# Performance work log

Measured on AMD Instinct MI355X. Metric: run time of the kernel, lower is better.

Reference implementation:

```python
import jax, jax.numpy as jnp
import numpy as np

EMB = 2048; H = 32; G = 8; D = 64; GS = H // G; EPS = 1e-6

def _rmsnorm(x, scale):
    x32 = x.astype(jnp.float32)
    var = jnp.mean(x32 * x32, axis=-1, keepdims=True)
    return (x32 * jax.lax.rsqrt(var + EPS) * scale).astype(x.dtype)

def _rope(x, cos, sin):
    # x: [B, h, S, D]; cos/sin: [S, D]
    d = x.shape[-1]
    x1, x2 = x[..., : d // 2], x[..., d // 2 :]
    rot = jnp.concatenate([-x2, x1], axis=-1)
    return (x * cos[None, None] + rot * sin[None, None]).astype(x.dtype)

def setup_inputs() -> dict:
    key = jax.random.key(0)
    ks = jax.random.split(key, 6)
    B, S = 2, 2048
    x = jax.random.normal(ks[0], (B, S, EMB), jnp.float32)
    # causal mask: True = blocked (masked_fill semantics)
    mask = jnp.triu(jnp.ones((S, S), dtype=bool), k=1)
    # standard RoPE tables, half-dim rotation, shape [S, D]
    inv_freq = 1.0 / (10000.0 ** (jnp.arange(0, D, 2, dtype=jnp.float32) / D))
    ang = jnp.arange(S, dtype=jnp.float32)[:, None] * inv_freq[None, :]  # [S, D/2]
    cos = jnp.concatenate([jnp.cos(ang), jnp.cos(ang)], axis=-1)
    sin = jnp.concatenate([jnp.sin(ang), jnp.sin(ang)], axis=-1)
    Wq = jax.random.normal(ks[1], (EMB, H * D), jnp.float32) * 0.02
    Wk = jax.random.normal(ks[2], (EMB, G * D), jnp.float32) * 0.02
    Wv = jax.random.normal(ks[3], (EMB, G * D), jnp.float32) * 0.02
    Wo = jax.random.normal(ks[4], (H * D, EMB), jnp.float32) * 0.02
    q_scale = jnp.ones((D,), jnp.float32)
    k_scale = jnp.ones((D,), jnp.float32)
    return {"x": x, "mask": mask, "cos": cos, "sin": sin, "Wq": Wq, "Wk": Wk,
            "Wv": Wv, "Wo": Wo, "q_scale": q_scale, "k_scale": k_scale}

def reference(x, mask, cos, sin, Wq, Wk, Wv, Wo, q_scale, k_scale):
    B, S, _ = x.shape
    q = (x @ Wq).reshape(B, S, H, D).transpose(0, 2, 1, 3)  # [B,H,S,D]
    k = (x @ Wk).reshape(B, S, G, D).transpose(0, 2, 1, 3)  # [B,G,S,D]
    v = (x @ Wv).reshape(B, S, G, D).transpose(0, 2, 1, 3)
    q = _rmsnorm(q, q_scale)
    k = _rmsnorm(k, k_scale)
    q = _rope(q, cos, sin)
    k = _rope(k, cos, sin)
    # GQA expansion (repeat_interleave over head dim)
    k = jnp.repeat(k, GS, axis=1)
    v = jnp.repeat(v, GS, axis=1)
    scale = 1.0 / np.float32(np.sqrt(D))
    s = jnp.einsum('bhqd,bhkd->bhqk', q.astype(jnp.float32), k.astype(jnp.float32)) * scale
    # flash path is causal regardless of `mask` arg; mask here equals causal
    s = jnp.where(mask[None, None], -jnp.inf, s)
    w = jax.nn.softmax(s, axis=-1)
    ctx = jnp.einsum('bhqk,bhkd->bhqd', w, v.astype(jnp.float32))
    ctx = ctx.transpose(0, 2, 1, 3).reshape(B, S, H * D)
    return ctx @ Wo
```

## Files before the change

### kernel.cpp

```cpp
#include <hip/hip_runtime.h>
#include <hip/hip_bf16.h>
#include <cstdint>
#include <cstddef>

#define EMB   2048
#define NH_   32
#define NG_   8
#define DH_   64
#define SEQ_  2048
#define BB_   2
#define MTOT  4096
#define LDQKV 3072
#define SM_C  0.18033688f

typedef __attribute__((ext_vector_type(8))) short s16x8;
typedef __attribute__((ext_vector_type(8))) unsigned short u16x8;
typedef __attribute__((ext_vector_type(4))) float f32x4;
typedef __attribute__((ext_vector_type(16))) float f32x16;
typedef __attribute__((ext_vector_type(4))) unsigned int u32x4;
typedef __attribute__((ext_vector_type(2))) unsigned int u32x2;
typedef __attribute__((ext_vector_type(2))) int i32x2;

__device__ __forceinline__ float bf2f(unsigned short u) {
  unsigned int x = (unsigned int)u << 16; return __uint_as_float(x);
}
__device__ __forceinline__ unsigned short f2bf(float f) {
  unsigned int x = __float_as_uint(f);
  x = x + 0x7FFFu + ((x >> 16) & 1u);
  return (unsigned short)(x >> 16);
}
__device__ __forceinline__ float ninf() { return __int_as_float(0xff800000); }
__device__ __forceinline__ unsigned int pack_bf2(float a, float b) {
  unsigned int r;
  asm("v_cvt_pk_bf16_f32 %0, %1, %2" : "=v"(r) : "v"(a), "v"(b));
  return r;
}
__device__ __forceinline__ void plswap(unsigned int& a, unsigned int& b) {
  i32x2 r = __builtin_amdgcn_permlane32_swap((int)a, (int)b, false, false);
  a = (unsigned int)r[0]; b = (unsigned int)r[1];
}
__device__ __forceinline__ void plswapf(float& a, float& b) {
  unsigned int ua = __float_as_uint(a), ub = __float_as_uint(b);
  plswap(ua, ub);
  a = __uint_as_float(ua); b = __uint_as_float(ub);
}

__device__ __forceinline__ void glds16(const void* g, void* l) {
  __builtin_amdgcn_global_load_lds((const __attribute__((address_space(1))) void*)g,
                                   (__attribute__((address_space(3))) void*)l, 16, 0, 0);
}

__device__ __forceinline__ void hw_sincos(float ang, float& c, float& s) {
  float rev = ang * 0.15915494309f;
  rev = rev - floorf(rev);
  asm("v_cos_f32 %0, %1" : "=v"(c) : "v"(rev));
  asm("v_sin_f32 %0, %1" : "=v"(s) : "v"(rev));
}

__global__ __launch_bounds__(256)
void prep(const float* __restrict__ x, const float* __restrict__ Wq,
          const float* __restrict__ Wk, const float* __restrict__ Wv,
          const float* __restrict__ Wo, unsigned short* __restrict__ xb,
          unsigned short* __restrict__ Wt, unsigned short* __restrict__ Wot) {
  __shared__ float tile[64][65];
  const int tid = threadIdx.x;
  const int bid = blockIdx.x;
  if (bid < 4096) {
    size_t i = (size_t)bid * 256 + tid;
    float4 a = *(const float4*)(x + i * 8);
    float4 c = *(const float4*)(x + i * 8 + 4);
    u16x8 o;
    o[0] = f2bf(a.x); o[1] = f2bf(a.y); o[2] = f2bf(a.z); o[3] = f2bf(a.w);
    o[4] = f2bf(c.x); o[5] = f2bf(c.y); o[6] = f2bf(c.z); o[7] = f2bf(c.w);
    *(u16x8*)(xb + i * 8) = o;
    return;
  }
  const float* in; unsigned short* out; int N; int local;
  if (bid < 5120)      { in = Wq; out = Wt;                       N = 2048; local = bid - 4096; }
  else if (bid < 5376) { in = Wk; out = Wt + (size_t)2048 * 2048; N = 512;  local = bid - 5120; }
  else if (bid < 5632) { in = Wv; out = Wt + (size_t)2560 * 2048; N = 512;  local = bid - 5376; }
  else                 { in = Wo; out = Wot;                      N = 2048; local = bid - 5632; }
  const int ntile = N >> 6;
  const int n0 = (local % ntile) * 64, k0 = (local / ntile) * 64;
  #pragma unroll
  for (int jj = 0; jj < 4; ++jj) {
    int r = (tid >> 4) + jj * 16;
    int c = (tid & 15) * 4;
    float4 v = *(const float4*)(in + (size_t)(k0 + r) * N + n0 + c);
    tile[r][c] = v.x; tile[r][c + 1] = v.y; tile[r][c + 2] = v.z; tile[r][c + 3] = v.w;
  }
  __syncthreads();
  #pragma unroll
  for (int rep = 0; rep < 2; ++rep) {
    int u = rep * 256 + tid;
    int nl = u >> 3, ch = u & 7;
    u16x8 o;
    #pragma unroll
    for (int e = 0; e < 8; ++e) o[e] = f2bf(tile[ch * 8 + e][nl]);
    *(u16x8*)(out + (size_t)(n0 + nl) * 2048 + k0 + ch * 8) = o;
  }
}

template<int BN, int F32OUT>
__global__ __launch_bounds__(512, 1)
void gemm256(const unsigned short* __restrict__ A, const unsigned short* __restrict__ Bt,
             void* __restrict__ C, int ldc) {
  constexpr int BUF = 16384 + BN * 64;
  constexpr int WN = BN / 64;
  constexpr int RW = 256 / (8 / WN);
  __shared__ __align__(16) char L[4][BUF];
  const int tid = threadIdx.x;
  const int wid = tid >> 6, lane = tid & 63;
  const int wm = wid / WN, wn = wid % WN;
  const int grp = lane >> 4, l15 = lane & 15;
  const int bm = blockIdx.y * 256, bn = blockIdx.x * BN;
  const int nt = 64;

  const int srow = tid >> 2;
  const int sc = (tid & 3) ^ ((srow >> 1) & 3);
  const int grp2 = grp ^ ((l15 >> 1) & 3);

  auto stage_ht = [&](int t, int h) {
    const unsigned short* src = (h < 2)
      ? A  + (size_t)(bm + h * 128 + srow) * 2048 + t * 32 + sc * 8
      : Bt + (size_t)(bn + (h - 2) * 128 + srow) * 2048 + t * 32 + sc * 8;
    glds16(src, &L[t & 3][h * 8192 + wid * 1024]);
  };

  constexpr int NST = 2 + BN / 128;
  f32x4 acc[RW / 16][4] = {};

  #pragma unroll
  for (int h = 0; h < NST; ++h) stage_ht(0, h);
  #pragma unroll
  for (int h = 0; h < NST; ++h) stage_ht(1, h);
  if constexpr (BN == 256) asm volatile("s_waitcnt vmcnt(4)" ::: "memory");
  else                     asm volatile("s_waitcnt vmcnt(3)" ::: "memory");
  __builtin_amdgcn_sched_barrier(0);
  __builtin_amdgcn_s_barrier();
  __builtin_amdgcn_sched_barrier(0);

  for (int t = 0; t < nt; ++t) {
    const char* Ab = &L[t & 3][0]     + (size_t)(wm * RW + l15) * 64 + grp2 * 16;
    const char* Bb = &L[t & 3][16384] + (size_t)(wn * 64 + l15) * 64 + grp2 * 16;
    const bool pre = (t + 2 < nt);
    if (pre) { stage_ht(t + 2, 0); stage_ht(t + 2, 1); }
    s16x8 bf[4], af[4];
    #pragma unroll
    for (int j = 0; j < 4; ++j) bf[j] = *(const s16x8*)(Bb + j * 1024);
    #pragma unroll
    for (int i = 0; i < 4; ++i) af[i] = *(const s16x8*)(Ab + i * 1024);
    __builtin_amdgcn_s_setprio(1);
    #pragma unroll
    for (int i = 0; i < 4; ++i)
      #pragma unroll
      for (int j = 0; j < 4; ++j)
        acc[i][j] = __builtin_amdgcn_mfma_f32_16x16x32_bf16(af[i], bf[j], acc[i][j], 0, 0, 0);
    __builtin_amdgcn_s_setprio(0);
    if constexpr (BN == 256) {
      if (pre) { stage_ht(t + 2, 2); stage_ht(t + 2, 3); }
      #pragma unroll
      for (int i = 0; i < 4; ++i) af[i] = *(const s16x8*)(Ab + (4 + i) * 1024);
      __builtin_amdgcn_s_setprio(1);
      #pragma unroll
      for (int i = 0; i < 4; ++i)
        #pragma unroll
        for (int j = 0; j < 4; ++j)
          acc[4 + i][j] = __builtin_amdgcn_mfma_f32_16x16x32_bf16(af[i], bf[j], acc[4 + i][j], 0, 0, 0);
      __builtin_amdgcn_s_setprio(0);
    } else {
      if (pre) stage_ht(t + 2, 2);
    }
    if (t + 1 < nt) {
      if (pre) {
        if constexpr (BN == 256) asm volatile("s_waitcnt vmcnt(4)" ::: "memory");
        else                     asm volatile("s_waitcnt vmcnt(3)" ::: "memory");
      } else {
        asm volatile("s_waitcnt vmcnt(0)" ::: "memory");
      }
      __builtin_amdgcn_sched_barrier(0);
      __builtin_amdgcn_s_barrier();
      __builtin_amdgcn_sched_barrier(0);
    }
  }

  #pragma unroll
  for (int i = 0; i < RW / 16; ++i)
    #pragma unroll
    for (int j = 0; j < 4; ++j)
      #pragma unroll
      for (int r = 0; r < 4; ++r) {
        int row = bm + wm * RW + i * 16 + grp * 4 + r;
        int col = bn + wn * 64 + j * 16 + l15;
        float v = acc[i][j][r];
        if (F32OUT) ((float*)C)[(size_t)row * ldc + col] = v;
        else        ((unsigned short*)C)[(size_t)row * ldc + col] = f2bf(v);
      }
}

__global__ __launch_bounds__(256)
void kvtile_rms(const unsigned short* __restrict__ qkv, const float* __restrict__ ksc,
                const float* __restrict__ cs, const float* __restrict__ sn,
                unsigned short* __restrict__ Kt, unsigned short* __restrict__ Vt) {
  __shared__ unsigned short Kl[32][72];
  __shared__ unsigned short Vl[32][72];
  const int tid = threadIdx.x;
  const int kt = blockIdx.x;
  const int bg = blockIdx.y;
  const int b = bg >> 3, g = bg & 7;
  {
    const int row = tid >> 3, ch = tid & 7;
    const int spos = kt * 32 + row;
    u16x8 kv = *(const u16x8*)(qkv + (size_t)(b * SEQ_ + spos) * LDQKV + 2048 + g * 64 + ch * 8);
    float v[8]; float sq = 0.f;
    #pragma unroll
    for (int e = 0; e < 8; ++e) { v[e] = bf2f(kv[e]); sq += v[e] * v[e]; }
    sq += __shfl_xor(sq, 1); sq += __shfl_xor(sq, 2); sq += __shfl_xor(sq, 4);
    const float rn = rsqrtf(sq * (1.f / 64.f) + 1e-6f);
    float xn[8];
    #pragma unroll
    for (int e = 0; e < 8; ++e) xn[e] = v[e] * rn * ksc[ch * 8 + e];
    float pn[8];
    #pragma unroll
    for (int e = 0; e < 8; ++e) pn[e] = __shfl_xor(xn[e], 4);
    const bool lo = (ch < 4);
    #pragma unroll
    for (int e = 0; e < 8; ++e) {
      int d = ch * 8 + e;
      float c = cs[spos * 64 + d], si = sn[spos * 64 + d];
      float o = lo ? (xn[e] * c - pn[e] * si) : fmaf(xn[e], c, pn[e] * si);
      Kl[row][d] = f2bf(o);
    }
    u16x8 vv = *(const u16x8*)(qkv + (size_t)(b * SEQ_ + spos) * LDQKV + 2560 + g * 64 + ch * 8);
    #pragma unroll
    for (int e = 0; e < 8; ++e) Vl[row][ch * 8 + e] = vv[e];
  }
  __syncthreads();
  {
    int c = tid >> 5, row = tid & 31;
    u16x8 o;
    #pragma unroll
    for (int e = 0; e < 8; ++e) o[e] = Kl[row][c * 8 + e];
    *(u16x8*)(Kt + (((size_t)(bg * 64 + kt)) << 11) + (c * 32 + row) * 8) = o;
  }
  {
    int c = tid >> 6, d = tid & 63;
    u16x8 o;
    #pragma unroll
    for (int e = 0; e < 8; ++e) o[e] = Vl[c * 8 + e][d];
    *(u16x8*)(Vt + (((size_t)(bg * 64 + kt)) << 11) + (c * 64 + d) * 8) = o;
  }
}

__global__ __launch_bounds__(256)
void attn_mfma14(const unsigned short* __restrict__ qkv, const float* __restrict__ qsc,
                 const unsigned short* __restrict__ Ktg, const unsigned short* __restrict__ Vtg,
                 unsigned short* __restrict__ ctx) {
  __shared__ __align__(16) unsigned short LR[16 * 1024];
  const int tid = threadIdx.x;
  const int w = tid >> 6, lane = tid & 63;
  const int l31 = lane & 31, half = lane >> 5;
  const int bid = blockIdx.x;
  const int x8 = bid & 7, r = bid >> 3;
  const int bg = x8 + 8 * (r & 1);
  const int rr = r >> 1;
  const int slot = rr >> 4, gi = rr & 15;
  const int qt = (slot == 0) ? (63 - gi) : (slot == 1) ? gi
               : (slot == 2) ? (47 - gi) : (16 + gi);
  const int b = bg >> 3, g = bg & 7, h = g * 4 + w;
  const int qbase = qt * 32;
  const int nkt = qt + 1;

  s16x8 qf[4];
  {
    const int spos = qbase + l31;
    float qv[4][8]; float sq = 0.f;
    #pragma unroll
    for (int s2 = 0; s2 < 4; ++s2) {
      u16x8 raw = *(const u16x8*)(qkv + (size_t)(b * SEQ_ + spos) * LDQKV + h * 64 + half * 8 + s2 * 16);
      #pragma unroll
      for (int e = 0; e < 8; ++e) { qv[s2][e] = bf2f(raw[e]); sq += qv[s2][e] * qv[s2][e]; }
    }
    sq += __shfl_xor(sq, 32);
    const float rn = rsqrtf(sq * (1.f / 64.f) + 1e-6f);
    float xn[4][8];
    #pragma unroll
    for (int s2 = 0; s2 < 4; ++s2)
      #pragma unroll
      for (int e = 0; e < 8; ++e) xn[s2][e] = qv[s2][e] * rn * qsc[s2 * 16 + half * 8 + e];
    const float fs = (float)spos;
    float qo[4][8];
    #pragma unroll
    for (int s2 = 0; s2 < 2; ++s2)
      #pragma unroll
      for (int e = 0; e < 8; ++e) {
        int d = s2 * 16 + half * 8 + e;
        float invf = exp2f((float)d * -0.4152410119f);
        float c0, s0;
        hw_sincos(fs * invf, c0, s0);
        qo[s2][e]     = (xn[s2][e] * c0 - xn[s2 + 2][e] * s0) * SM_C;
        qo[s2 + 2][e] = fmaf(xn[s2 + 2][e], c0, xn[s2][e] * s0) * SM_C;
      }
    #pragma unroll
    for (int s2 = 0; s2 < 4; ++s2) {
      u32x4 t;
      t[0] = pack_bf2(qo[s2][0], qo[s2][1]); t[1] = pack_bf2(qo[s2][2], qo[s2][3]);
      t[2] = pack_bf2(qo[s2][4], qo[s2][5]); t[3] = pack_bf2(qo[s2][6], qo[s2][7]);
      qf[s2] = __builtin_bit_cast(s16x8, t);
    }
  }

  f32x16 acc0 = {}, acc1 = {};
  float l_st = 0.f;

  const size_t tbase = ((size_t)(bg * 64)) << 11;
  const int soff = (w << 9) + lane * 8;

  auto stage = [&](int kt_) {
    if (kt_ < nkt) {
      char* dst = (char*)LR + (kt_ & 3) * 8192;
      glds16(Ktg + tbase + ((size_t)kt_ << 11) + soff, dst + (w << 10));
      glds16(Vtg + tbase + ((size_t)kt_ << 11) + soff, dst + 4096 + (w << 10));
    }
  };

  auto body = [&](int kt_) {
    const char* Kb = (const char*)LR + (kt_ & 3) * 8192;
    const char* Vb = Kb + 4096;
    s16x8 KF0 = *(const s16x8*)(Kb + (((0 + half) << 5) + l31) * 16);
    s16x8 KF1 = *(const s16x8*)(Kb + (((2 + half) << 5) + l31) * 16);
    s16x8 KF2 = *(const s16x8*)(Kb + (((4 + half) << 5) + l31) * 16);
    s16x8 KF3 = *(const s16x8*)(Kb + (((6 + half) << 5) + l31) * 16);
    s16x8 vf00 = *(const s16x8*)(Vb + (((half) << 6) + l31) * 16);
    s16x8 vf01 = *(const s16x8*)(Vb + (((2 + half) << 6) + l31) * 16);
    s16x8 vf10 = *(const s16x8*)(Vb + (((half) << 6) + 32 + l31) * 16);
    s16x8 vf11 = *(const s16x8*)(Vb + (((2 + half) << 6) + 32 + l31) * 16);
    f32x16 st = {};
    __builtin_amdgcn_s_setprio(1);
    st = __builtin_amdgcn_mfma_f32_32x32x16_bf16(KF0, qf[0], st, 0, 0, 0);
    st = __builtin_amdgcn_mfma_f32_32x32x16_bf16(KF1, qf[1], st, 0, 0, 0);
    st = __builtin_amdgcn_mfma_f32_32x32x16_bf16(KF2, qf[2], st, 0, 0, 0);
    st = __builtin_amdgcn_mfma_f32_32x32x16_bf16(KF3, qf[3], st, 0, 0, 0);
    __builtin_amdgcn_s_setprio(0);
    if (kt_ == qt) {
      #pragma unroll
      for (int r2 = 0; r2 < 16; ++r2) {
        int key = (r2 & 3) + 8 * (r2 >> 2) + 4 * half;
        if (key > l31) st[r2] = ninf();
      }
    }
    float p[16];
    #pragma unroll
    for (int r2 = 0; r2 < 16; ++r2) p[r2] = exp2f(st[r2]);
    float s8[8];
    #pragma unroll
    for (int r2 = 0; r2 < 8; ++r2) s8[r2] = p[r2] + p[r2 + 8];
    float psum = ((s8[0] + s8[1]) + (s8[2] + s8[3])) + ((s8[4] + s8[5]) + (s8[6] + s8[7]));
    { float a2 = psum, b2 = psum; plswapf(a2, b2); psum = a2 + b2; }
    l_st += psum;
    unsigned int PK[8];
    #pragma unroll
    for (int j2 = 0; j2 < 8; ++j2) PK[j2] = pack_bf2(p[2 * j2], p[2 * j2 + 1]);
    plswap(PK[0], PK[2]); plswap(PK[1], PK[3]);
    plswap(PK[4], PK[6]); plswap(PK[5], PK[7]);
    u32x4 pb0u, pb1u;
    pb0u[0] = PK[0]; pb0u[1] = PK[1]; pb0u[2] = PK[2]; pb0u[3] = PK[3];
    pb1u[0] = PK[4]; pb1u[1] = PK[5]; pb1u[2] = PK[6]; pb1u[3] = PK[7];
    s16x8 pb0 = __builtin_bit_cast(s16x8, pb0u);
    s16x8 pb1 = __builtin_bit_cast(s16x8, pb1u);
    __builtin_amdgcn_s_setprio(1);
    acc0 = __builtin_amdgcn_mfma_f32_32x32x16_bf16(vf00, pb0, acc0, 0, 0, 0);
    acc1 = __builtin_amdgcn_mfma_f32_32x32x16_bf16(vf10, pb0, acc1, 0, 0, 0);
    acc0 = __builtin_amdgcn_mfma_f32_32x32x16_bf16(vf01, pb1, acc0, 0, 0, 0);
    acc1 = __builtin_amdgcn_mfma_f32_32x32x16_bf16(vf11, pb1, acc1, 0, 0, 0);
    __builtin_amdgcn_s_setprio(0);
  };

  stage(0);
  stage(1);
  for (int t = 0; t < nkt; ++t) {
    if (t + 1 < nkt) asm volatile("s_waitcnt vmcnt(2)" ::: "memory");
    else             asm volatile("s_waitcnt vmcnt(0)" ::: "memory");
    __builtin_amdgcn_sched_barrier(0);
    __builtin_amdgcn_s_barrier();
    __builtin_amdgcn_sched_barrier(0);
    stage(t + 2);
    body(t);
  }

  const float linv = 1.f / l_st;
  unsigned short* orow = ctx + (size_t)(b * SEQ_ + qbase + l31) * 2048 + h * 64;
  #pragma unroll
  for (int dt = 0; dt < 2; ++dt) {
    #pragma unroll
    for (int rq = 0; rq < 4; ++rq) {
      const int rr2 = rq * 4;
      const int d0 = dt * 32 + 8 * rq + 4 * half;
      float a0 = (dt ? acc1[rr2]     : acc0[rr2])     * linv;
      float a1 = (dt ? acc1[rr2 + 1] : acc0[rr2 + 1]) * linv;
      float a2 = (dt ? acc1[rr2 + 2] : acc0[rr2 + 2]) * linv;
      float a3 = (dt ? acc1[rr2 + 3] : acc0[rr2 + 3]) * linv;
      u32x2 o;
      o[0] = pack_bf2(a0, a1);
      o[1] = pack_bf2(a2, a3);
      *(u32x2*)(orow + d0) = o;
    }
  }
}

extern "C" void kernel_launch(void* const* d_in, const int* in_sizes, int n_in,
                              void* d_out, int out_size, void* d_ws, size_t ws_size,
                              hipStream_t stream) {
  const float* x  = (const float*)d_in[0];
  const float* cs = (const float*)d_in[2];
  const float* sn = (const float*)d_in[3];
  const float* Wq = (const float*)d_in[4];
  const float* Wk = (const float*)d_in[5];
  const float* Wv = (const float*)d_in[6];
  const float* Wo = (const float*)d_in[7];
  const float* qs = (const float*)d_in[8];
  const float* ks = (const float*)d_in[9];
  float* out = (float*)d_out;

  unsigned short* xb  = (unsigned short*)d_ws;
  unsigned short* Wt  = xb  + (size_t)4096 * 2048;
  unsigned short* Wot = Wt  + (size_t)3072 * 2048;
  unsigned short* qkv = Wot + (size_t)2048 * 2048;
  unsigned short* vTb = qkv + (size_t)4096 * 3072;
  unsigned short* ctx = vTb + (size_t)16 * 64 * 2048;
  unsigned short* Ktt = xb;

  prep<<<6656, 256, 0, stream>>>(x, Wq, Wk, Wv, Wo, xb, Wt, Wot);
  gemm256<256, 0><<<dim3(12, 16), 512, 0, stream>>>(xb, Wt, qkv, 3072);
  kvtile_rms<<<dim3(64, 16), 256, 0, stream>>>(qkv, ks, cs, sn, Ktt, vTb);
  attn_mfma14<<<1024, 256, 0, stream>>>(qkv, qs, Ktt, vTb, ctx);
  gemm256<128, 1><<<dim3(16, 16), 512, 0, stream>>>(ctx, Wot, out, 2048);
}
```

Baseline: 186.6 us.

## Split attention blocks to two heads each with a double-buffered K/V pipeline

```diff
diff --git a/kernel.cpp b/kernel.cpp
--- a/kernel.cpp
+++ b/kernel.cpp
@@ -252,22 +252,24 @@
   }
 }
 
-__global__ __launch_bounds__(256)
-void attn_mfma14(const unsigned short* __restrict__ qkv, const float* __restrict__ qsc,
+__global__ __launch_bounds__(128)
+void attn_mfma15(const unsigned short* __restrict__ qkv, const float* __restrict__ qsc,
                  const unsigned short* __restrict__ Ktg, const unsigned short* __restrict__ Vtg,
                  unsigned short* __restrict__ ctx) {
-  __shared__ __align__(16) unsigned short LR[16 * 1024];
+  __shared__ __align__(16) unsigned short LA[4 * 1024];
+  __shared__ __align__(16) unsigned short LB[4 * 1024];
   const int tid = threadIdx.x;
   const int w = tid >> 6, lane = tid & 63;
   const int l31 = lane & 31, half = lane >> 5;
   const int bid = blockIdx.x;
   const int x8 = bid & 7, r = bid >> 3;
-  const int bg = x8 + 8 * (r & 1);
-  const int rr = r >> 1;
-  const int slot = rr >> 4, gi = rr & 15;
+  const int v = r & 7, u = r >> 3;
+  const int hp = v & 1, slot = v >> 1;
+  const int bgl = u >> 4, gi = u & 15;
+  const int bg = x8 + 8 * bgl;
   const int qt = (slot == 0) ? (63 - gi) : (slot == 1) ? gi
                : (slot == 2) ? (47 - gi) : (16 + gi);
-  const int b = bg >> 3, g = bg & 7, h = g * 4 + w;
+  const int b = bg >> 3, g = bg & 7, h = g * 4 + hp * 2 + w;
   const int qbase = qt * 32;
   const int nkt = qt + 1;
 
@@ -314,18 +316,19 @@
   float l_st = 0.f;
 
   const size_t tbase = ((size_t)(bg * 64)) << 11;
-  const int soff = (w << 9) + lane * 8;
-
-  auto stage = [&](int kt_) {
-    if (kt_ < nkt) {
-      char* dst = (char*)LR + (kt_ & 3) * 8192;
-      glds16(Ktg + tbase + ((size_t)kt_ << 11) + soff, dst + (w << 10));
-      glds16(Vtg + tbase + ((size_t)kt_ << 11) + soff, dst + 4096 + (w << 10));
+
+  auto stage = [&](unsigned short* Lb, int kt_) {
+    const size_t toff = tbase + ((size_t)kt_ << 11);
+    #pragma unroll
+    for (int q = 0; q < 2; ++q) {
+      const int so = (w * 2 + q) * 512 + lane * 8;
+      glds16(Ktg + toff + so, (char*)Lb + (w * 2 + q) * 1024);
+      glds16(Vtg + toff + so, (char*)Lb + 4096 + (w * 2 + q) * 1024);
     }
   };
 
-  auto body = [&](int kt_) {
-    const char* Kb = (const char*)LR + (kt_ & 3) * 8192;
+  auto body = [&](const unsigned short* Lb, int kt_) {
+    const char* Kb = (const char*)Lb;
     const char* Vb = Kb + 4096;
     s16x8 KF0 = *(const s16x8*)(Kb + (((0 + half) << 5) + l31) * 16);
     s16x8 KF1 = *(const s16x8*)(Kb + (((2 + half) << 5) + l31) * 16);
@@ -376,16 +379,17 @@
     __builtin_amdgcn_s_setprio(0);
   };
 
-  stage(0);
-  stage(1);
-  for (int t = 0; t < nkt; ++t) {
-    if (t + 1 < nkt) asm volatile("s_waitcnt vmcnt(2)" ::: "memory");
-    else             asm volatile("s_waitcnt vmcnt(0)" ::: "memory");
-    __builtin_amdgcn_sched_barrier(0);
-    __builtin_amdgcn_s_barrier();
-    __builtin_amdgcn_sched_barrier(0);
-    stage(t + 2);
-    body(t);
+  stage(LA, 0);
+  int kt = 0;
+  while (true) {
+    __syncthreads();
+    if (kt + 1 < nkt) stage(LB, kt + 1);
+    body(LA, kt);
+    ++kt; if (kt >= nkt) break;
+    __syncthreads();
+    if (kt + 1 < nkt) stage(LA, kt + 1);
+    body(LB, kt);
+    ++kt; if (kt >= nkt) break;
   }
 
   const float linv = 1.f / l_st;
@@ -433,6 +437,6 @@
   prep<<<6656, 256, 0, stream>>>(x, Wq, Wk, Wv, Wo, xb, Wt, Wot);
   gemm256<256, 0><<<dim3(12, 16), 512, 0, stream>>>(xb, Wt, qkv, 3072);
   kvtile_rms<<<dim3(64, 16), 256, 0, stream>>>(qkv, ks, cs, sn, Ktt, vTb);
-  attn_mfma14<<<1024, 256, 0, stream>>>(qkv, qs, Ktt, vTb, ctx);
+  attn_mfma15<<<2048, 128, 0, stream>>>(qkv, qs, Ktt, vTb, ctx);
   gemm256<128, 1><<<dim3(16, 16), 512, 0, stream>>>(ctx, Wot, out, 2048);
 }
```

Result: slower. 230.3 us (+23.4%).

## Split KV tiles across two wave groups in attention with LDS reduction

Applied to the files above, without the earlier changes.

```diff
diff --git a/kernel.cpp b/kernel.cpp
--- a/kernel.cpp
+++ b/kernel.cpp
@@ -252,13 +252,15 @@
   }
 }
 
-__global__ __launch_bounds__(256)
-void attn_mfma14(const unsigned short* __restrict__ qkv, const float* __restrict__ qsc,
+__global__ __launch_bounds__(512)
+void attn_mfma16(const unsigned short* __restrict__ qkv, const float* __restrict__ qsc,
                  const unsigned short* __restrict__ Ktg, const unsigned short* __restrict__ Vtg,
                  unsigned short* __restrict__ ctx) {
-  __shared__ __align__(16) unsigned short LR[16 * 1024];
+  __shared__ __align__(16) char SM[2][2][8192];
+  __shared__ float Lx[256];
   const int tid = threadIdx.x;
   const int w = tid >> 6, lane = tid & 63;
+  const int gw = w >> 2, lw = w & 3;
   const int l31 = lane & 31, half = lane >> 5;
   const int bid = blockIdx.x;
   const int x8 = bid & 7, r = bid >> 3;
@@ -267,9 +269,10 @@
   const int slot = rr >> 4, gi = rr & 15;
   const int qt = (slot == 0) ? (63 - gi) : (slot == 1) ? gi
                : (slot == 2) ? (47 - gi) : (16 + gi);
-  const int b = bg >> 3, g = bg & 7, h = g * 4 + w;
+  const int b = bg >> 3, g = bg & 7, h = g * 4 + lw;
   const int qbase = qt * 32;
   const int nkt = qt + 1;
+  const int niter = (nkt + 1) >> 1;
 
   s16x8 qf[4];
   {
@@ -314,18 +317,19 @@
   float l_st = 0.f;
 
   const size_t tbase = ((size_t)(bg * 64)) << 11;
-  const int soff = (w << 9) + lane * 8;
-
-  auto stage = [&](int kt_) {
+  const int soff = (lw << 9) + lane * 8;
+
+  auto stage = [&](int buf, int i) {
+    const int kt_ = 2 * i + gw;
     if (kt_ < nkt) {
-      char* dst = (char*)LR + (kt_ & 3) * 8192;
-      glds16(Ktg + tbase + ((size_t)kt_ << 11) + soff, dst + (w << 10));
-      glds16(Vtg + tbase + ((size_t)kt_ << 11) + soff, dst + 4096 + (w << 10));
+      const size_t toff = tbase + ((size_t)kt_ << 11);
+      glds16(Ktg + toff + soff, &SM[gw][buf][lw << 10]);
+      glds16(Vtg + toff + soff, &SM[gw][buf][4096 + (lw << 10)]);
     }
   };
 
-  auto body = [&](int kt_) {
-    const char* Kb = (const char*)LR + (kt_ & 3) * 8192;
+  auto body = [&](int buf, int kt_) {
+    const char* Kb = &SM[gw][buf][0];
     const char* Vb = Kb + 4096;
     s16x8 KF0 = *(const s16x8*)(Kb + (((0 + half) << 5) + l31) * 16);
     s16x8 KF1 = *(const s16x8*)(Kb + (((2 + half) << 5) + l31) * 16);
@@ -376,34 +380,47 @@
     __builtin_amdgcn_s_setprio(0);
   };
 
-  stage(0);
-  stage(1);
-  for (int t = 0; t < nkt; ++t) {
-    if (t + 1 < nkt) asm volatile("s_waitcnt vmcnt(2)" ::: "memory");
-    else             asm volatile("s_waitcnt vmcnt(0)" ::: "memory");
-    __builtin_amdgcn_sched_barrier(0);
-    __builtin_amdgcn_s_barrier();
-    __builtin_amdgcn_sched_barrier(0);
-    stage(t + 2);
-    body(t);
-  }
-
-  const float linv = 1.f / l_st;
-  unsigned short* orow = ctx + (size_t)(b * SEQ_ + qbase + l31) * 2048 + h * 64;
-  #pragma unroll
-  for (int dt = 0; dt < 2; ++dt) {
-    #pragma unroll
-    for (int rq = 0; rq < 4; ++rq) {
-      const int rr2 = rq * 4;
-      const int d0 = dt * 32 + 8 * rq + 4 * half;
-      float a0 = (dt ? acc1[rr2]     : acc0[rr2])     * linv;
-      float a1 = (dt ? acc1[rr2 + 1] : acc0[rr2 + 1]) * linv;
-      float a2 = (dt ? acc1[rr2 + 2] : acc0[rr2 + 2]) * linv;
-      float a3 = (dt ? acc1[rr2 + 3] : acc0[rr2 + 3]) * linv;
-      u32x2 o;
-      o[0] = pack_bf2(a0, a1);
-      o[1] = pack_bf2(a2, a3);
-      *(u32x2*)(orow + d0) = o;
+  stage(0, 0);
+  int buf = 0;
+  for (int i = 0; i < niter; ++i) {
+    __syncthreads();
+    if (i + 1 < niter) stage(buf ^ 1, i + 1);
+    const int kt_ = 2 * i + gw;
+    if (kt_ < nkt) body(buf, kt_);
+    buf ^= 1;
+  }
+
+  __syncthreads();
+  float* MF = (float*)&SM[0][0][0];
+  if (gw == 1) {
+    const int base = (lw * 64 + lane) * 32;
+    #pragma unroll
+    for (int r2 = 0; r2 < 16; ++r2) { MF[base + r2] = acc0[r2]; MF[base + 16 + r2] = acc1[r2]; }
+    Lx[lw * 64 + lane] = l_st;
+  }
+  __syncthreads();
+  if (gw == 0) {
+    const int base = (lw * 64 + lane) * 32;
+    #pragma unroll
+    for (int r2 = 0; r2 < 16; ++r2) { acc0[r2] += MF[base + r2]; acc1[r2] += MF[base + 16 + r2]; }
+    l_st += Lx[lw * 64 + lane];
+    const float linv = 1.f / l_st;
+    unsigned short* orow = ctx + (size_t)(b * SEQ_ + qbase + l31) * 2048 + h * 64;
+    #pragma unroll
+    for (int dt = 0; dt < 2; ++dt) {
+      #pragma unroll
+      for (int rq = 0; rq < 4; ++rq) {
+        const int rr2 = rq * 4;
+        const int d0 = dt * 32 + 8 * rq + 4 * half;
+        float a0 = (dt ? acc1[rr2]     : acc0[rr2])     * linv;
+        float a1 = (dt ? acc1[rr2 + 1] : acc0[rr2 + 1]) * linv;
+        float a2 = (dt ? acc1[rr2 + 2] : acc0[rr2 + 2]) * linv;
+        float a3 = (dt ? acc1[rr2 + 3] : acc0[rr2 + 3]) * linv;
+        u32x2 o;
+        o[0] = pack_bf2(a0, a1);
+        o[1] = pack_bf2(a2, a3);
+        *(u32x2*)(orow + d0) = o;
+      }
     }
   }
 }
@@ -433,6 +450,6 @@
   prep<<<6656, 256, 0, stream>>>(x, Wq, Wk, Wv, Wo, xb, Wt, Wot);
   gemm256<256, 0><<<dim3(12, 16), 512, 0, stream>>>(xb, Wt, qkv, 3072);
   kvtile_rms<<<dim3(64, 16), 256, 0, stream>>>(qkv, ks, cs, sn, Ktt, vTb);
-  attn_mfma14<<<1024, 256, 0, stream>>>(qkv, qs, Ktt, vTb, ctx);
+  attn_mfma16<<<1024, 512, 0, stream>>>(qkv, qs, Ktt, vTb, ctx);
   gemm256<128, 1><<<dim3(16, 16), 512, 0, stream>>>(ctx, Wot, out, 2048);
 }
```

After: 192.8 us. 3.3% more time.
